# Kernel optimization log

Hardware: AMD Instinct MI355X
Metric: run time of the kernel (lower is better)

Reference implementation:

```python
import jax, jax.numpy as jnp
import numpy as np

E, H, I, T, K = 8, 2048, 1024, 4096, 2
GROUP = 32


def dequant_int4(packed, scale, group):
    """packed: [E, R, C//2] ints in [0,256) holding two 4-bit values per byte.
    scale: [E, R, C//group]. Returns fp32 [E, R, C] with w = (nibble - 8) * scale."""
    lo = (packed & 0xF) - 8          # even columns
    hi = ((packed >> 4) & 0xF) - 8   # odd columns
    e, r, ch = packed.shape
    w = jnp.stack([lo, hi], axis=-1).reshape(e, r, 2 * ch).astype(jnp.float32)
    w = w.reshape(e, r, -1, group) * scale[..., None]
    return w.reshape(e, r, 2 * ch)


def setup_inputs() -> dict:
    key = jax.random.key(0)
    ks = jax.random.split(key, 6)
    x = jax.random.normal(ks[0], (T, H), dtype=jnp.float32)
    w1 = jax.random.randint(ks[1], (E, 2 * I, H // 2), 0, 256, dtype=jnp.int32)
    w1_scale = jax.random.uniform(ks[2], (E, 2 * I, H // GROUP), dtype=jnp.float32) * 0.02
    w2 = jax.random.randint(ks[3], (E, H, I // 2), 0, 256, dtype=jnp.int32)
    w2_scale = jax.random.uniform(ks[4], (E, H, I // GROUP), dtype=jnp.float32) * 0.02
    logits = jax.random.normal(ks[5], (T, E), dtype=jnp.float32)
    top_vals, top_idx = jax.lax.top_k(logits, K)
    expert_weights = jax.nn.softmax(top_vals, axis=-1)   # [T, K]
    expert_indices = top_idx.astype(jnp.int32)           # [T, K]
    return {"x": x, "w1": w1, "w1_scale": w1_scale, "w2": w2,
            "w2_scale": w2_scale, "expert_weights": expert_weights,
            "expert_indices": expert_indices, "top_k": K}


def reference(x, w1, w1_scale, w2, w2_scale, expert_weights, expert_indices, top_k):
    inter = w2.shape[2] * 2
    W1 = dequant_int4(w1, w1_scale, GROUP)   # [E, 2I, H]
    W2 = dequant_int4(w2, w2_scale, GROUP)   # [E, H, I]
    y13 = jnp.einsum('th,erh->etr', x, W1)   # [E, T, 2I]
    gate, up = y13[..., :inter], y13[..., inter:]
    h = jax.nn.silu(gate) * up               # [E, T, I] SwiGLU
    y = jnp.einsum('eti,ehi->eth', h, W2)    # [E, T, H]
    t_ids = jnp.arange(x.shape[0])[:, None]  # [T, 1]
    sel = y[expert_indices, t_ids, :]        # [T, K, H]
    return jnp.einsum('tkh,tk->th', sel, expert_weights)
```

## Files before the change

kernel.cpp:

```cpp
#include <hip/hip_runtime.h>
#include <cstdint>
#include <cstddef>

typedef unsigned int u32;
typedef unsigned short u16;
typedef __bf16 bf16x8 __attribute__((ext_vector_type(8)));
typedef float f32x4 __attribute__((ext_vector_type(4)));
typedef u16 u16x8 __attribute__((ext_vector_type(8)));

static constexpr int T_TOK = 4096;
static constexpr int HID   = 2048;
static constexpr int INTER = 1024;
static constexpr int NEXP  = 8;
static constexpr int TOPK  = 2;
static constexpr int SLOT_CAP = 10240;
static constexpr int NT_M = SLOT_CAP / 256;

static constexpr int META_TOK = 32;
static constexpr int META_SLOTOF = 32 + SLOT_CAP;

__device__ __forceinline__ u16 f2bf(float f) {
  u32 u = __builtin_bit_cast(u32, f);
  u32 r = (u + 0x7fffu + ((u >> 16) & 1u)) >> 16;
  return (u16)r;
}
__device__ __forceinline__ float bf2f(u16 h) {
  return __builtin_bit_cast(float, (u32)h << 16);
}

__global__ void router_count(const int* __restrict__ eidx, int* __restrict__ meta) {
  __shared__ int cnt[NEXP];
  const int tid = threadIdx.x;
  if (tid < NEXP) cnt[tid] = 0;
  __syncthreads();
  for (int i = tid; i < T_TOK * TOPK; i += 256) atomicAdd(&cnt[eidx[i]], 1);
  __syncthreads();
  if (tid == 0) {
    int off = 0;
    for (int e = 0; e < NEXP; ++e) {
      int c = cnt[e];
      meta[e] = c;
      meta[8 + e] = off;
      meta[17 + e] = off;
      off += (c + 255) & ~255;
    }
    meta[16] = off;
  }
}

__global__ void toklist_init(int* __restrict__ meta) {
  const int i = blockIdx.x * 256 + threadIdx.x;
  if (i < SLOT_CAP) meta[META_TOK + i] = 0;
}

__global__ void router_assign(const int* __restrict__ eidx, int* __restrict__ meta) {
  const int t = blockIdx.x * 256 + threadIdx.x;
  if (t >= T_TOK) return;
  int* cursors = meta + 17;
  int* toklist = meta + META_TOK;
  int* slot_of = meta + META_SLOTOF;
  for (int k = 0; k < TOPK; ++k) {
    const int e = eidx[t * TOPK + k];
    const int pos = atomicAdd(&cursors[e], 1);
    toklist[pos] = t;
    slot_of[t * TOPK + k] = pos;
  }
}

template <int CPR>
__global__ void dequant_k(const int* __restrict__ p, const float* __restrict__ s,
                          u16* __restrict__ w) {
  const int gid = blockIdx.x * 256 + threadIdx.x;
  const int row = gid / CPR;
  const int cid = gid % CPR;
  const int4 pk = *(const int4*)(p + (size_t)gid * 4);
  const float sc = s[(size_t)row * (CPR / 4) + (cid >> 2)];
  int v[4] = {pk.x, pk.y, pk.z, pk.w};
  u16x8 o;
#pragma unroll
  for (int b = 0; b < 4; ++b) {
    o[2 * b]     = f2bf((float)((v[b] & 15) - 8) * sc);
    o[2 * b + 1] = f2bf((float)(((v[b] >> 4) & 15) - 8) * sc);
  }
  *(u16x8*)(w + (size_t)gid * 8) = o;
}

__global__ void cast_x_k(const float* __restrict__ x, u16* __restrict__ xb) {
  const int i = (blockIdx.x * 256 + threadIdx.x) * 8;
  const float4 a = *(const float4*)(x + i);
  const float4 b = *(const float4*)(x + i + 4);
  u16x8 o;
  o[0] = f2bf(a.x); o[1] = f2bf(a.y); o[2] = f2bf(a.z); o[3] = f2bf(a.w);
  o[4] = f2bf(b.x); o[5] = f2bf(b.y); o[6] = f2bf(b.z); o[7] = f2bf(b.w);
  *(u16x8*)(xb + i) = o;
}

template <int KT, bool GATHER, bool GUP>
__global__ __launch_bounds__(512, 2) void gemm256(const u16* __restrict__ A,
                                                  const u16* __restrict__ B,
                                                  u16* __restrict__ Cout,
                                                  const int* __restrict__ meta) {
  static constexpr int NT = KT / 64;
  static constexpr int OSTR = GUP ? INTER : HID;

  const int bid = blockIdx.x;
  const int mt = bid % NT_M;
  const int nt = bid / NT_M;
  const int slot0 = mt * 256;
  if (slot0 >= meta[16]) return;
  int e = 0;
#pragma unroll
  for (int i = 1; i < NEXP; ++i) e += (slot0 >= meta[8 + i]);
  const int tid = threadIdx.x;

  __shared__ u16 lds[2 * 32768];
  char* ldsB = (char*)lds;

  const u16* Be = B + (size_t)e * 2048 * KT;
  const int* toklist = meta + META_TOK;

  const u16* asrc[4];
  const u16* bsrc[4];
#pragma unroll
  for (int j = 0; j < 4; ++j) {
    const int L = j * 8192 + tid * 16;
    const int S = L >> 10;
    int o = L & 1023;
    o ^= ((o >> 8) & 3) << 4;
    const int r = (S >> 1) * 16 + (o >> 6);
    const int cb = (S & 1) * 64 + (o & 63);
    const int arow = GATHER ? toklist[slot0 + r] : (slot0 + r);
    asrc[j] = A + (size_t)arow * KT + (cb >> 1);
    int brow;
    if (GUP) {
      const int g = r >> 6, j6 = r & 63;
      brow = nt * 128 + g * 32 + (j6 & 31) + ((j6 >> 5) << 10);
    } else {
      brow = nt * 256 + r;
    }
    bsrc[j] = Be + (size_t)brow * KT + (cb >> 1);
  }

#define STAGE(kt_, c_)                                                                \
  do {                                                                                \
    char* dA_ = ldsB + (c_) * 65536;                                                  \
    char* dB_ = dA_ + 32768;                                                          \
    _Pragma("unroll") for (int j = 0; j < 4; ++j)                                     \
        __builtin_amdgcn_global_load_lds(                                             \
            (const __attribute__((address_space(1))) void*)(asrc[j] + (kt_) * 64),    \
            (__attribute__((address_space(3))) void*)(dA_ + j * 8192 + tid * 16),     \
            16, 0, 0);                                                                \
    _Pragma("unroll") for (int j = 0; j < 4; ++j)                                     \
        __builtin_amdgcn_global_load_lds(                                             \
            (const __attribute__((address_space(1))) void*)(bsrc[j] + (kt_) * 64),    \
            (__attribute__((address_space(3))) void*)(dB_ + j * 8192 + tid * 16),     \
            16, 0, 0);                                                                \
  } while (0)

  const int lane = tid & 63;
  const int wid = tid >> 6;
  const int wm = (wid >> 2) * 128;
  const int wn = (wid & 3) * 64;
  const int fr = lane & 15;
  const int qq = lane >> 4;
  const int swz = (qq * 16) ^ (((fr >> 2) & 3) << 4);

  int aoff[2][4][2], boff[4][2];
#pragma unroll
  for (int mh = 0; mh < 2; ++mh)
#pragma unroll
    for (int mf = 0; mf < 4; ++mf)
#pragma unroll
      for (int ks = 0; ks < 2; ++ks)
        aoff[mh][mf][ks] = ((wm + mh * 64 + mf * 16) >> 4) * 2048 + ks * 1024 + fr * 64 + swz;
#pragma unroll
  for (int nf = 0; nf < 4; ++nf)
#pragma unroll
    for (int ks = 0; ks < 2; ++ks)
      boff[nf][ks] = 32768 + ((wn + nf * 16) >> 4) * 2048 + ks * 1024 + fr * 64 + swz;

  f32x4 acc[8][4];
#pragma unroll
  for (int m = 0; m < 8; ++m)
#pragma unroll
    for (int n = 0; n < 4; ++n) acc[m][n] = (f32x4)0.0f;

#define COMPUTE(c_)                                                                   \
  do {                                                                                \
    const char* bb_ = ldsB + (c_) * 65536;                                            \
    bf16x8 bfr_[4][2];                                                                \
    _Pragma("unroll") for (int nf = 0; nf < 4; ++nf)                                  \
        _Pragma("unroll") for (int ks = 0; ks < 2; ++ks)                              \
            bfr_[nf][ks] = *(const bf16x8*)(bb_ + boff[nf][ks]);                      \
    _Pragma("unroll") for (int mh = 0; mh < 2; ++mh) {                                \
      bf16x8 af_[4][2];                                                               \
      _Pragma("unroll") for (int mf = 0; mf < 4; ++mf)                                \
          _Pragma("unroll") for (int ks = 0; ks < 2; ++ks)                            \
              af_[mf][ks] = *(const bf16x8*)(bb_ + aoff[mh][mf][ks]);                 \
      __builtin_amdgcn_s_setprio(1);                                                  \
      _Pragma("unroll") for (int mf = 0; mf < 4; ++mf)                                \
          _Pragma("unroll") for (int nf = 0; nf < 4; ++nf)                            \
              _Pragma("unroll") for (int ks = 0; ks < 2; ++ks)                        \
                  acc[mh * 4 + mf][nf] = __builtin_amdgcn_mfma_f32_16x16x32_bf16(     \
                      af_[mf][ks], bfr_[nf][ks], acc[mh * 4 + mf][nf], 0, 0, 0);      \
      __builtin_amdgcn_s_setprio(0);                                                  \
    }                                                                                 \
  } while (0)

  STAGE(0, 0);
#pragma unroll 1
  for (int kt = 0; kt < NT; kt += 2) {
    asm volatile("s_waitcnt vmcnt(0)" ::: "memory");
    __builtin_amdgcn_s_barrier();
    __builtin_amdgcn_sched_barrier(0);
    if (kt + 1 < NT) STAGE(kt + 1, 1);
    COMPUTE(0);
    asm volatile("s_waitcnt vmcnt(0)" ::: "memory");
    __builtin_amdgcn_s_barrier();
    __builtin_amdgcn_sched_barrier(0);
    if (kt + 2 < NT) STAGE(kt + 2, 0);
    COMPUTE(1);
  }
#undef STAGE
#undef COMPUTE

  if (GUP) {
    const int g = wid & 3;
#pragma unroll
    for (int mi = 0; mi < 8; ++mi)
#pragma unroll
      for (int n = 0; n < 2; ++n)
#pragma unroll
        for (int jj = 0; jj < 4; ++jj) {
          const float gv = acc[mi][n][jj];
          const float uv = acc[mi][n + 2][jj];
          const float hv = gv / (1.0f + __expf(-gv)) * uv;
          const int row = slot0 + wm + mi * 16 + qq * 4 + jj;
          Cout[(size_t)row * OSTR + nt * 128 + g * 32 + n * 16 + fr] = f2bf(hv);
        }
  } else {
#pragma unroll
    for (int mi = 0; mi < 8; ++mi)
#pragma unroll
      for (int n = 0; n < 4; ++n)
#pragma unroll
        for (int jj = 0; jj < 4; ++jj) {
          const int row = slot0 + wm + mi * 16 + qq * 4 + jj;
          const int col = nt * 256 + wn + n * 16 + fr;
          Cout[(size_t)row * OSTR + col] = f2bf(acc[mi][n][jj]);
        }
  }
}

__global__ void combine_k(const u16* __restrict__ yp, const float* __restrict__ ew,
                          const int* __restrict__ meta, float* __restrict__ out) {
  const int idx = blockIdx.x * 256 + threadIdx.x;
  const int t = idx >> 8;
  const int pos = (idx & 255) * 8;
  const int* slot_of = meta + META_SLOTOF;
  const int s0 = slot_of[t * 2];
  const int s1 = slot_of[t * 2 + 1];
  const float w0 = ew[t * 2];
  const float w1 = ew[t * 2 + 1];
  const u16x8 v0 = *(const u16x8*)(yp + (size_t)s0 * 2048 + pos);
  const u16x8 v1 = *(const u16x8*)(yp + (size_t)s1 * 2048 + pos);
  float* dst = out + (size_t)t * 2048 + pos;
  float4 o0, o1;
  o0.x = w0 * bf2f(v0[0]) + w1 * bf2f(v1[0]);
  o0.y = w0 * bf2f(v0[1]) + w1 * bf2f(v1[1]);
  o0.z = w0 * bf2f(v0[2]) + w1 * bf2f(v1[2]);
  o0.w = w0 * bf2f(v0[3]) + w1 * bf2f(v1[3]);
  o1.x = w0 * bf2f(v0[4]) + w1 * bf2f(v1[4]);
  o1.y = w0 * bf2f(v0[5]) + w1 * bf2f(v1[5]);
  o1.z = w0 * bf2f(v0[6]) + w1 * bf2f(v1[6]);
  o1.w = w0 * bf2f(v0[7]) + w1 * bf2f(v1[7]);
  *(float4*)dst = o0;
  *(float4*)(dst + 4) = o1;
}

extern "C" void kernel_launch(void* const* d_in, const int* in_sizes, int n_in,
                              void* d_out, int out_size, void* d_ws, size_t ws_size,
                              hipStream_t stream) {
  const float* x    = (const float*)d_in[0];
  const int*   w1   = (const int*)d_in[1];
  const float* w1s  = (const float*)d_in[2];
  const int*   w2   = (const int*)d_in[3];
  const float* w2s  = (const float*)d_in[4];
  const float* ew   = (const float*)d_in[5];
  const int*   eidx = (const int*)d_in[6];
  float* out = (float*)d_out;

  char* ws = (char*)d_ws;
  const size_t OFF_W1B  = 0;
  const size_t OFF_W2B  = 67108864;
  const size_t OFF_XB   = 100663296;
  const size_t OFF_H    = 117440512;
  const size_t OFF_META = 138412032;
  const size_t NEED     = 138485888;
  if (ws_size < NEED) return;

  u16* W1b  = (u16*)(ws + OFF_W1B);
  u16* yp   = (u16*)(ws + OFF_W1B);
  u16* W2b  = (u16*)(ws + OFF_W2B);
  u16* xb   = (u16*)(ws + OFF_XB);
  u16* hbuf = (u16*)(ws + OFF_H);
  int* meta = (int*)(ws + OFF_META);

  router_count<<<1, 256, 0, stream>>>(eidx, meta);
  toklist_init<<<SLOT_CAP / 256, 256, 0, stream>>>(meta);
  router_assign<<<T_TOK / 256, 256, 0, stream>>>(eidx, meta);

  cast_x_k<<<(T_TOK * HID) / (256 * 8), 256, 0, stream>>>(x, xb);
  dequant_k<256><<<16384 * 256 / 256, 256, 0, stream>>>(w1, w1s, W1b);
  dequant_k<128><<<16384 * 128 / 256, 256, 0, stream>>>(w2, w2s, W2b);

  gemm256<2048, true, true><<<NT_M * 8, 512, 0, stream>>>(xb, W1b, hbuf, meta);
  gemm256<1024, false, false><<<NT_M * 8, 512, 0, stream>>>(hbuf, W2b, yp, meta);

  combine_k<<<(T_TOK * HID) / (256 * 8), 256, 0, stream>>>(yp, ew, meta, out);
}
```

Baseline: 278.9 us.

## Interleave global-to-LDS loads with MFMA sub-phases in a ping-pong pipeline

Replaces the two-stage loop (wait for all loads, barrier, stage next tile, compute) with a finer schedule. Each k-tile's compute is split into four MFMA quarters, with LDS fragment reads, partial global_load_lds issues and barriers placed between them. vmcnt waits are relaxed to partial counts so loads stay in flight across compute. Precomputed LDS offset arrays are replaced by base plus immediate offsets to save registers. The cost is many more barriers. The wraparound load indices (masking with NT-1) also issue redundant loads on the final iterations and assume NT is a power of two.

```diff
diff --git a/kernel.cpp b/kernel.cpp
--- a/kernel.cpp
+++ b/kernel.cpp
@@ -141,21 +141,18 @@
     bsrc[j] = Be + (size_t)brow * KT + (cb >> 1);
   }
 
-#define STAGE(kt_, c_)                                                                \
-  do {                                                                                \
-    char* dA_ = ldsB + (c_) * 65536;                                                  \
-    char* dB_ = dA_ + 32768;                                                          \
-    _Pragma("unroll") for (int j = 0; j < 4; ++j)                                     \
-        __builtin_amdgcn_global_load_lds(                                             \
-            (const __attribute__((address_space(1))) void*)(asrc[j] + (kt_) * 64),    \
-            (__attribute__((address_space(3))) void*)(dA_ + j * 8192 + tid * 16),     \
-            16, 0, 0);                                                                \
-    _Pragma("unroll") for (int j = 0; j < 4; ++j)                                     \
-        __builtin_amdgcn_global_load_lds(                                             \
-            (const __attribute__((address_space(1))) void*)(bsrc[j] + (kt_) * 64),    \
-            (__attribute__((address_space(3))) void*)(dB_ + j * 8192 + tid * 16),     \
-            16, 0, 0);                                                                \
-  } while (0)
+#define STG_A(kt_, c_, j_)                                                          \
+  __builtin_amdgcn_global_load_lds(                                                 \
+      (const __attribute__((address_space(1))) void*)(asrc[j_] + (kt_) * 64),       \
+      (__attribute__((address_space(3))) void*)(ldsB + (c_) * 65536 + (j_) * 8192 + \
+                                                tid * 16),                           \
+      16, 0, 0)
+#define STG_B(kt_, c_, j_)                                                          \
+  __builtin_amdgcn_global_load_lds(                                                 \
+      (const __attribute__((address_space(1))) void*)(bsrc[j_] + (kt_) * 64),       \
+      (__attribute__((address_space(3))) void*)(ldsB + (c_) * 65536 + 32768 +       \
+                                                (j_) * 8192 + tid * 16),             \
+      16, 0, 0)
 
   const int lane = tid & 63;
   const int wid = tid >> 6;
@@ -165,19 +162,8 @@
   const int qq = lane >> 4;
   const int swz = (qq * 16) ^ (((fr >> 2) & 3) << 4);
 
-  int aoff[2][4][2], boff[4][2];
-#pragma unroll
-  for (int mh = 0; mh < 2; ++mh)
-#pragma unroll
-    for (int mf = 0; mf < 4; ++mf)
-#pragma unroll
-      for (int ks = 0; ks < 2; ++ks)
-        aoff[mh][mf][ks] = ((wm + mh * 64 + mf * 16) >> 4) * 2048 + ks * 1024 + fr * 64 + swz;
-#pragma unroll
-  for (int nf = 0; nf < 4; ++nf)
-#pragma unroll
-    for (int ks = 0; ks < 2; ++ks)
-      boff[nf][ks] = 32768 + ((wn + nf * 16) >> 4) * 2048 + ks * 1024 + fr * 64 + swz;
+  const int abase = (wm >> 4) * 2048 + fr * 64 + swz;
+  const int bbase = 32768 + (wn >> 4) * 2048 + fr * 64 + swz;
 
   f32x4 acc[8][4];
 #pragma unroll
@@ -185,44 +171,77 @@
 #pragma unroll
     for (int n = 0; n < 4; ++n) acc[m][n] = (f32x4)0.0f;
 
-#define COMPUTE(c_)                                                                   \
-  do {                                                                                \
-    const char* bb_ = ldsB + (c_) * 65536;                                            \
-    bf16x8 bfr_[4][2];                                                                \
-    _Pragma("unroll") for (int nf = 0; nf < 4; ++nf)                                  \
-        _Pragma("unroll") for (int ks = 0; ks < 2; ++ks)                              \
-            bfr_[nf][ks] = *(const bf16x8*)(bb_ + boff[nf][ks]);                      \
-    _Pragma("unroll") for (int mh = 0; mh < 2; ++mh) {                                \
-      bf16x8 af_[4][2];                                                               \
-      _Pragma("unroll") for (int mf = 0; mf < 4; ++mf)                                \
-          _Pragma("unroll") for (int ks = 0; ks < 2; ++ks)                            \
-              af_[mf][ks] = *(const bf16x8*)(bb_ + aoff[mh][mf][ks]);                 \
-      __builtin_amdgcn_s_setprio(1);                                                  \
-      _Pragma("unroll") for (int mf = 0; mf < 4; ++mf)                                \
-          _Pragma("unroll") for (int nf = 0; nf < 4; ++nf)                            \
-              _Pragma("unroll") for (int ks = 0; ks < 2; ++ks)                        \
-                  acc[mh * 4 + mf][nf] = __builtin_amdgcn_mfma_f32_16x16x32_bf16(     \
-                      af_[mf][ks], bfr_[nf][ks], acc[mh * 4 + mf][nf], 0, 0, 0);      \
-      __builtin_amdgcn_s_setprio(0);                                                  \
-    }                                                                                 \
+  bf16x8 af[4][2], b01[2][2], b23[2][2];
+
+#define BARRIER asm volatile("s_barrier" ::: "memory")
+#define LGKM0                                              \
+  do {                                                     \
+    asm volatile("s_waitcnt lgkmcnt(0)" ::: "memory");     \
+    __builtin_amdgcn_sched_barrier(0);                     \
   } while (0)
 
-  STAGE(0, 0);
+#define DS_AF(c_, mh_)                                                              \
+  _Pragma("unroll") for (int mf = 0; mf < 4; ++mf)                                  \
+  _Pragma("unroll") for (int ks = 0; ks < 2; ++ks)                                  \
+      af[mf][ks] = *(const bf16x8*)(ldsB + (c_) * 65536 + abase + (mh_) * 8192 +    \
+                                    mf * 2048 + ks * 1024);
+#define DS_B(c_, bh_, BV_)                                                          \
+  _Pragma("unroll") for (int nf = 0; nf < 2; ++nf)                                  \
+  _Pragma("unroll") for (int ks = 0; ks < 2; ++ks)                                  \
+      BV_[nf][ks] = *(const bf16x8*)(ldsB + (c_) * 65536 + bbase +                  \
+                                     ((bh_) * 2 + nf) * 2048 + ks * 1024);
+#define MFMA16(mh_, bh_, BV_)                                                       \
+  do {                                                                              \
+    __builtin_amdgcn_s_setprio(1);                                                  \
+    _Pragma("unroll") for (int mf = 0; mf < 4; ++mf)                                \
+    _Pragma("unroll") for (int nf = 0; nf < 2; ++nf)                                \
+    _Pragma("unroll") for (int ks = 0; ks < 2; ++ks)                                \
+        acc[(mh_) * 4 + mf][(bh_) * 2 + nf] =                                       \
+            __builtin_amdgcn_mfma_f32_16x16x32_bf16(                                \
+                af[mf][ks], BV_[nf][ks], acc[(mh_) * 4 + mf][(bh_) * 2 + nf],       \
+                0, 0, 0);                                                           \
+    __builtin_amdgcn_s_setprio(0);                                                  \
+  } while (0)
+
+  STG_A(0, 0, 0); STG_A(0, 0, 2); STG_B(0, 0, 0); STG_B(0, 0, 1);
+  STG_B(0, 0, 2); STG_B(0, 0, 3); STG_A(0, 0, 1); STG_A(0, 0, 3);
+  STG_A(1, 1, 0); STG_A(1, 1, 2); STG_B(1, 1, 0); STG_B(1, 1, 1);
+  STG_B(1, 1, 2); STG_B(1, 1, 3); STG_A(1, 1, 1); STG_A(1, 1, 3);
+  asm volatile("s_waitcnt vmcnt(8)" ::: "memory");
+  BARRIER;
+
 #pragma unroll 1
-  for (int kt = 0; kt < NT; kt += 2) {
-    asm volatile("s_waitcnt vmcnt(0)" ::: "memory");
-    __builtin_amdgcn_s_barrier();
-    __builtin_amdgcn_sched_barrier(0);
-    if (kt + 1 < NT) STAGE(kt + 1, 1);
-    COMPUTE(0);
-    asm volatile("s_waitcnt vmcnt(0)" ::: "memory");
-    __builtin_amdgcn_s_barrier();
-    __builtin_amdgcn_sched_barrier(0);
-    if (kt + 2 < NT) STAGE(kt + 2, 0);
-    COMPUTE(1);
-  }
-#undef STAGE
-#undef COMPUTE
+  for (int it = 0; it < NT / 2; ++it) {
+    const int s0 = (2 * it + 2) & (NT - 1);
+    const int s1 = (2 * it + 3) & (NT - 1);
+    DS_AF(0, 0); DS_B(0, 0, b01);
+    BARRIER; LGKM0; MFMA16(0, 0, b01); BARRIER;
+    DS_B(0, 1, b23); STG_A(s0, 0, 0); STG_A(s0, 0, 2);
+    BARRIER; LGKM0; MFMA16(0, 1, b23); BARRIER;
+    DS_AF(0, 1); STG_B(s0, 0, 0); STG_B(s0, 0, 1);
+    BARRIER; LGKM0; MFMA16(1, 0, b01); BARRIER;
+    STG_B(s0, 0, 2); STG_B(s0, 0, 3);
+    BARRIER; MFMA16(1, 1, b23);
+    asm volatile("s_waitcnt vmcnt(6)" ::: "memory");
+    BARRIER;
+    DS_AF(1, 0); DS_B(1, 0, b01); STG_A(s0, 0, 1); STG_A(s0, 0, 3);
+    BARRIER; LGKM0; MFMA16(0, 0, b01); BARRIER;
+    DS_B(1, 1, b23); STG_A(s1, 1, 0); STG_A(s1, 1, 2);
+    BARRIER; LGKM0; MFMA16(0, 1, b23); BARRIER;
+    DS_AF(1, 1); STG_B(s1, 1, 0); STG_B(s1, 1, 1); STG_B(s1, 1, 2); STG_B(s1, 1, 3);
+    BARRIER; LGKM0; MFMA16(1, 0, b01); BARRIER;
+    STG_A(s1, 1, 1); STG_A(s1, 1, 3);
+    BARRIER; MFMA16(1, 1, b23);
+    asm volatile("s_waitcnt vmcnt(8)" ::: "memory");
+    BARRIER;
+  }
+#undef STG_A
+#undef STG_B
+#undef BARRIER
+#undef LGKM0
+#undef DS_AF
+#undef DS_B
+#undef MFMA16
 
   if (GUP) {
     const int g = wid & 3;
```

Measured after the change: 288.6 us. 3.5% more time.

## Merge both expert GEMMs into one persistent kernel with work queue and dependencies

Applied to the files above, without the earlier changes.

Replaces the two separate GEMM launches with a persistent kernel of 256 workgroups that pull tiles from an atomic queue. Phase-1 tiles come first; a phase-2 tile for an M-tile waits on per-M-tile completion counters, or on a global counter if the workspace is too small to give yp its own buffer. The goal is to overlap the tail of the first GEMM with the start of the second and to remove the launch gap. The LDS swizzle pattern and the fragment address computation also change. This adds spin-waiting, atomics, and a risk of deadlock if not all workgroups are co-resident.

```diff
diff --git a/kernel.cpp b/kernel.cpp
--- a/kernel.cpp
+++ b/kernel.cpp
@@ -14,10 +14,17 @@
 static constexpr int NEXP  = 8;
 static constexpr int TOPK  = 2;
 static constexpr int SLOT_CAP = 10240;
-static constexpr int NT_M = SLOT_CAP / 256;
-
-static constexpr int META_TOK = 32;
-static constexpr int META_SLOTOF = 32 + SLOT_CAP;
+static constexpr int NT_M = 40;
+static constexpr int N_G = 320;
+
+static constexpr int M_TOT   = 16;
+static constexpr int M_CUR   = 17;
+static constexpr int M_Q     = 25;
+static constexpr int M_G1ALL = 26;
+static constexpr int M_DONE  = 40;
+static constexpr int M_TOK   = 96;
+static constexpr int M_SLOTOF = 96 + SLOT_CAP;
+static constexpr int META_INTS = 96 + SLOT_CAP + T_TOK * TOPK;
 
 __device__ __forceinline__ u16 f2bf(float f) {
   u32 u = __builtin_bit_cast(u32, f);
@@ -26,6 +33,18 @@
 }
 __device__ __forceinline__ float bf2f(u16 h) {
   return __builtin_bit_cast(float, (u32)h << 16);
+}
+
+__device__ __forceinline__ void spin_ge(int* p, int target) {
+  while (__hip_atomic_load(p, __ATOMIC_ACQUIRE, __HIP_MEMORY_SCOPE_AGENT) < target)
+    __builtin_amdgcn_s_sleep(8);
+}
+__device__ __forceinline__ void bump(int* p, int tid) {
+  __syncthreads();
+  if (tid == 0) {
+    __threadfence();
+    __hip_atomic_fetch_add(p, 1, __ATOMIC_RELEASE, __HIP_MEMORY_SCOPE_AGENT);
+  }
 }
 
 __global__ void router_count(const int* __restrict__ eidx, int* __restrict__ meta) {
@@ -41,24 +60,25 @@
       int c = cnt[e];
       meta[e] = c;
       meta[8 + e] = off;
-      meta[17 + e] = off;
+      meta[M_CUR + e] = off;
       off += (c + 255) & ~255;
     }
-    meta[16] = off;
-  }
-}
-
-__global__ void toklist_init(int* __restrict__ meta) {
+    meta[M_TOT] = off;
+  }
+}
+
+__global__ void init_k(int* __restrict__ meta) {
   const int i = blockIdx.x * 256 + threadIdx.x;
-  if (i < SLOT_CAP) meta[META_TOK + i] = 0;
+  if (i < SLOT_CAP) meta[M_TOK + i] = 0;
+  if (i >= 25 && i < 80) meta[i] = 0;
 }
 
 __global__ void router_assign(const int* __restrict__ eidx, int* __restrict__ meta) {
   const int t = blockIdx.x * 256 + threadIdx.x;
   if (t >= T_TOK) return;
-  int* cursors = meta + 17;
-  int* toklist = meta + META_TOK;
-  int* slot_of = meta + META_SLOTOF;
+  int* cursors = meta + M_CUR;
+  int* toklist = meta + M_TOK;
+  int* slot_of = meta + M_SLOTOF;
   for (int k = 0; k < TOPK; ++k) {
     const int e = eidx[t * TOPK + k];
     const int pos = atomicAdd(&cursors[e], 1);
@@ -95,29 +115,13 @@
   *(u16x8*)(xb + i) = o;
 }
 
-template <int KT, bool GATHER, bool GUP>
-__global__ __launch_bounds__(512, 2) void gemm256(const u16* __restrict__ A,
-                                                  const u16* __restrict__ B,
-                                                  u16* __restrict__ Cout,
-                                                  const int* __restrict__ meta) {
+template <int KT, bool G1M>
+__device__ void gemm_body(const u16* __restrict__ A, const u16* __restrict__ Be,
+                          u16* __restrict__ Cout, const int* __restrict__ toklist,
+                          u16* lds, int slot0, int nt, int tid) {
   static constexpr int NT = KT / 64;
-  static constexpr int OSTR = GUP ? INTER : HID;
-
-  const int bid = blockIdx.x;
-  const int mt = bid % NT_M;
-  const int nt = bid / NT_M;
-  const int slot0 = mt * 256;
-  if (slot0 >= meta[16]) return;
-  int e = 0;
-#pragma unroll
-  for (int i = 1; i < NEXP; ++i) e += (slot0 >= meta[8 + i]);
-  const int tid = threadIdx.x;
-
-  __shared__ u16 lds[2 * 32768];
+  static constexpr int OSTR = G1M ? INTER : HID;
   char* ldsB = (char*)lds;
-
-  const u16* Be = B + (size_t)e * 2048 * KT;
-  const int* toklist = meta + META_TOK;
 
   const u16* asrc[4];
   const u16* bsrc[4];
@@ -126,13 +130,13 @@
     const int L = j * 8192 + tid * 16;
     const int S = L >> 10;
     int o = L & 1023;
-    o ^= ((o >> 8) & 3) << 4;
+    o ^= ((o >> 7) & 3) << 4;
     const int r = (S >> 1) * 16 + (o >> 6);
     const int cb = (S & 1) * 64 + (o & 63);
-    const int arow = GATHER ? toklist[slot0 + r] : (slot0 + r);
+    const int arow = G1M ? toklist[slot0 + r] : (slot0 + r);
     asrc[j] = A + (size_t)arow * KT + (cb >> 1);
     int brow;
-    if (GUP) {
+    if (G1M) {
       const int g = r >> 6, j6 = r & 63;
       brow = nt * 128 + g * 32 + (j6 & 31) + ((j6 >> 5) << 10);
     } else {
@@ -163,21 +167,10 @@
   const int wn = (wid & 3) * 64;
   const int fr = lane & 15;
   const int qq = lane >> 4;
-  const int swz = (qq * 16) ^ (((fr >> 2) & 3) << 4);
-
-  int aoff[2][4][2], boff[4][2];
-#pragma unroll
-  for (int mh = 0; mh < 2; ++mh)
-#pragma unroll
-    for (int mf = 0; mf < 4; ++mf)
-#pragma unroll
-      for (int ks = 0; ks < 2; ++ks)
-        aoff[mh][mf][ks] = ((wm + mh * 64 + mf * 16) >> 4) * 2048 + ks * 1024 + fr * 64 + swz;
-#pragma unroll
-  for (int nf = 0; nf < 4; ++nf)
-#pragma unroll
-    for (int ks = 0; ks < 2; ++ks)
-      boff[nf][ks] = 32768 + ((wn + nf * 16) >> 4) * 2048 + ks * 1024 + fr * 64 + swz;
+  const int swz = (qq * 16) ^ (((fr >> 1) & 3) << 4);
+
+  const int abase = (wm >> 4) * 2048 + fr * 64 + swz;
+  const int bbase = 32768 + (wn >> 4) * 2048 + fr * 64 + swz;
 
   f32x4 acc[8][4];
 #pragma unroll
@@ -191,12 +184,13 @@
     bf16x8 bfr_[4][2];                                                                \
     _Pragma("unroll") for (int nf = 0; nf < 4; ++nf)                                  \
         _Pragma("unroll") for (int ks = 0; ks < 2; ++ks)                              \
-            bfr_[nf][ks] = *(const bf16x8*)(bb_ + boff[nf][ks]);                      \
+            bfr_[nf][ks] = *(const bf16x8*)(bb_ + bbase + nf * 2048 + ks * 1024);     \
     _Pragma("unroll") for (int mh = 0; mh < 2; ++mh) {                                \
       bf16x8 af_[4][2];                                                               \
       _Pragma("unroll") for (int mf = 0; mf < 4; ++mf)                                \
           _Pragma("unroll") for (int ks = 0; ks < 2; ++ks)                            \
-              af_[mf][ks] = *(const bf16x8*)(bb_ + aoff[mh][mf][ks]);                 \
+              af_[mf][ks] = *(const bf16x8*)(bb_ + abase + mh * 8192 + mf * 2048 +    \
+                                             ks * 1024);                              \
       __builtin_amdgcn_s_setprio(1);                                                  \
       _Pragma("unroll") for (int mf = 0; mf < 4; ++mf)                                \
           _Pragma("unroll") for (int nf = 0; nf < 4; ++nf)                            \
@@ -224,7 +218,7 @@
 #undef STAGE
 #undef COMPUTE
 
-  if (GUP) {
+  if (G1M) {
     const int g = wid & 3;
 #pragma unroll
     for (int mi = 0; mi < 8; ++mi)
@@ -252,12 +246,57 @@
   }
 }
 
+__global__ __launch_bounds__(512, 2) void gemm_pers(
+    const u16* __restrict__ xb, const u16* __restrict__ W1b,
+    const u16* __restrict__ W2b, u16* __restrict__ hbuf, u16* __restrict__ yp,
+    int* __restrict__ meta, int gated) {
+  __shared__ u16 lds[2 * 32768];
+  __shared__ int sh_item;
+  const int tid = threadIdx.x;
+  const int* toklist = meta + M_TOK;
+
+  for (;;) {
+    __syncthreads();
+    if (tid == 0) sh_item = atomicAdd(&meta[M_Q], 1);
+    __syncthreads();
+    const int item = sh_item;
+    if (item >= 2 * N_G) return;
+
+    if (item < N_G) {
+      const int mt = item >> 3, nt = item & 7, slot0 = mt * 256;
+      if (slot0 < meta[M_TOT]) {
+        int e = 0;
+#pragma unroll
+        for (int i = 1; i < NEXP; ++i) e += (slot0 >= meta[8 + i]);
+        gemm_body<2048, true>(xb, W1b + (size_t)e * 2048 * 2048, hbuf, toklist,
+                              lds, slot0, nt, tid);
+        bump(&meta[M_DONE + mt], tid);
+      }
+      bump(&meta[M_G1ALL], tid);
+    } else {
+      const int t = item - N_G, mt = t >> 3, nt = t & 7, slot0 = mt * 256;
+      if (slot0 < meta[M_TOT]) {
+        int e = 0;
+#pragma unroll
+        for (int i = 1; i < NEXP; ++i) e += (slot0 >= meta[8 + i]);
+        if (tid == 0) {
+          if (gated) spin_ge(&meta[M_G1ALL], N_G);
+          else spin_ge(&meta[M_DONE + mt], 8);
+        }
+        __syncthreads();
+        gemm_body<1024, false>(hbuf, W2b + (size_t)e * 2048 * 1024, yp, toklist,
+                               lds, slot0, nt, tid);
+      }
+    }
+  }
+}
+
 __global__ void combine_k(const u16* __restrict__ yp, const float* __restrict__ ew,
                           const int* __restrict__ meta, float* __restrict__ out) {
   const int idx = blockIdx.x * 256 + threadIdx.x;
   const int t = idx >> 8;
   const int pos = (idx & 255) * 8;
-  const int* slot_of = meta + META_SLOTOF;
+  const int* slot_of = meta + M_SLOTOF;
   const int s0 = slot_of[t * 2];
   const int s1 = slot_of[t * 2 + 1];
   const float w0 = ew[t * 2];
@@ -296,26 +335,28 @@
   const size_t OFF_XB   = 100663296;
   const size_t OFF_H    = 117440512;
   const size_t OFF_META = 138412032;
-  const size_t NEED     = 138485888;
-  if (ws_size < NEED) return;
+  const size_t OFF_YP_A = 138488832;
+  const size_t NEED_B   = 138488832;
+  const size_t NEED_A   = 180431872;
+  if (ws_size < NEED_B) return;
+  const int gated = (ws_size < NEED_A) ? 1 : 0;
 
   u16* W1b  = (u16*)(ws + OFF_W1B);
-  u16* yp   = (u16*)(ws + OFF_W1B);
   u16* W2b  = (u16*)(ws + OFF_W2B);
   u16* xb   = (u16*)(ws + OFF_XB);
   u16* hbuf = (u16*)(ws + OFF_H);
   int* meta = (int*)(ws + OFF_META);
+  u16* yp   = gated ? (u16*)(ws + OFF_W1B) : (u16*)(ws + OFF_YP_A);
 
   router_count<<<1, 256, 0, stream>>>(eidx, meta);
-  toklist_init<<<SLOT_CAP / 256, 256, 0, stream>>>(meta);
+  init_k<<<SLOT_CAP / 256, 256, 0, stream>>>(meta);
   router_assign<<<T_TOK / 256, 256, 0, stream>>>(eidx, meta);
 
   cast_x_k<<<(T_TOK * HID) / (256 * 8), 256, 0, stream>>>(x, xb);
-  dequant_k<256><<<16384 * 256 / 256, 256, 0, stream>>>(w1, w1s, W1b);
-  dequant_k<128><<<16384 * 128 / 256, 256, 0, stream>>>(w2, w2s, W2b);
-
-  gemm256<2048, true, true><<<NT_M * 8, 512, 0, stream>>>(xb, W1b, hbuf, meta);
-  gemm256<1024, false, false><<<NT_M * 8, 512, 0, stream>>>(hbuf, W2b, yp, meta);
+  dequant_k<256><<<16384, 256, 0, stream>>>(w1, w1s, W1b);
+  dequant_k<128><<<8192, 256, 0, stream>>>(w2, w2s, W2b);
+
+  gemm_pers<<<256, 512, 0, stream>>>(xb, W1b, W2b, hbuf, yp, meta, gated);
 
   combine_k<<<(T_TOK * HID) / (256 * 8), 256, 0, stream>>>(yp, ew, meta, out);
 }
```

Measured after the change: 325.9 us. 1.17x slower.
